# Performance work log

Hardware: AMD Instinct MI355X
Metric: run time of the kernel (lower is better)

## Reference

```python
import jax, jax.numpy as jnp
import numpy as np

DIM = 1024
NUM_EXPERTS = 8
HIDDEN = 4096
CAP_FACTOR = 2.0
B, S = 4, 2048


def setup_inputs() -> dict:
    key = jax.random.key(0)
    ks = jax.random.split(key, 6)
    scale_r = 1.0 / np.sqrt(DIM)
    scale_1 = 1.0 / np.sqrt(DIM)
    scale_2 = 1.0 / np.sqrt(HIDDEN)
    return {
        "x": jax.random.normal(ks[0], (B, S, DIM), dtype=jnp.float32),
        # router: nn.Linear(dim, num_experts, bias=False) -> weight [E, D]
        "router_w": jax.random.uniform(ks[1], (NUM_EXPERTS, DIM), jnp.float32, -scale_r, scale_r),
        # stacked expert MLP params
        "w1": jax.random.uniform(ks[2], (NUM_EXPERTS, DIM, HIDDEN), jnp.float32, -scale_1, scale_1),
        "b1": jax.random.uniform(ks[3], (NUM_EXPERTS, HIDDEN), jnp.float32, -scale_1, scale_1),
        "w2": jax.random.uniform(ks[4], (NUM_EXPERTS, HIDDEN, DIM), jnp.float32, -scale_2, scale_2),
        "b2": jax.random.uniform(ks[5], (NUM_EXPERTS, DIM), jnp.float32, -scale_2, scale_2),
    }


def reference(x, router_w, w1, b1, w2, b2):
    # x: [B, S, D]
    Bz, Sz, Dz = x.shape
    E = router_w.shape[0]
    capacity = max(1, int(Sz * CAP_FACTOR / E) + 1)

    # router softmax over experts: [B, S, E]
    scores = jax.nn.softmax(jnp.einsum("bsd,ed->bse", x, router_w), axis=-1)

    # expert-choice: each expert picks top-C tokens. [B, E, S] -> [B, E, C]
    scores_t = jnp.swapaxes(scores, 1, 2)
    gate_vals, sel_idx = jax.lax.top_k(scores_t, capacity)

    # gather selected tokens: [B, E, C, D]
    b_idx = jnp.arange(Bz)[:, None, None]
    tokens = x[b_idx, sel_idx]

    # batched expert MLP (GELU exact, matching nn.GELU default)
    h = jnp.einsum("becd,edh->bech", tokens, w1) + b1[None, :, None, :]
    h = jax.nn.gelu(h, approximate=False)
    y = jnp.einsum("bech,ehd->becd", h, w2) + b2[None, :, None, :]

    # gate and scatter-add combine back to [B, S, D]
    gated = y * gate_vals[..., None]
    out = jnp.zeros_like(x).at[b_idx, sel_idx].add(gated)
    return out
```

## Files before the change

kernel.cpp:

```cpp
#include <hip/hip_runtime.h>
#include <cstdint>

#define DIMD  1024
#define NEXP  8
#define HIDN  4096
#define BATCH 4
#define SEQ   2048
#define CAPC  513
#define RPEX  2176
#define TPEX  17
#define MTOT  (NEXP * RPEX)
#define MTILES (MTOT / 128)

typedef __bf16 bf16x8 __attribute__((ext_vector_type(8)));
typedef float  f32x4  __attribute__((ext_vector_type(4)));

__device__ __forceinline__ unsigned short f2bf(float f) {
    unsigned u = __float_as_uint(f);
    unsigned r = (u + 0x7FFFu + ((u >> 16) & 1u)) >> 16;
    return (unsigned short)r;
}

__device__ __forceinline__ void swz_grp(int GY, int& bx, int& by) {
    int xcd = blockIdx.x & 7, pos = blockIdx.x >> 3;
    int tps = TPEX * GY;
    int sc = pos / tps, rem = pos - sc * tps;
    int bxl = rem / GY, byIn = rem - bxl * GY;
    bx = xcd * TPEX + bxl;
    by = sc * GY + byIn;
}

__global__ __launch_bounds__(64)
void router_kernel(const float* __restrict__ x, const float* __restrict__ rw,
                   float* __restrict__ scores) {
    int token = blockIdx.x;
    int lane  = threadIdx.x;
    const float4* xr = reinterpret_cast<const float4*>(x + (size_t)token * DIMD);
    float4 xv[4];
#pragma unroll
    for (int j = 0; j < 4; ++j) xv[j] = xr[lane * 4 + j];
    float acc[NEXP];
#pragma unroll
    for (int e = 0; e < NEXP; ++e) {
        const float4* wr = reinterpret_cast<const float4*>(rw + (size_t)e * DIMD);
        float a = 0.f;
#pragma unroll
        for (int j = 0; j < 4; ++j) {
            float4 wv = wr[lane * 4 + j];
            a += xv[j].x * wv.x; a += xv[j].y * wv.y;
            a += xv[j].z * wv.z; a += xv[j].w * wv.w;
        }
#pragma unroll
        for (int off = 32; off > 0; off >>= 1) a += __shfl_xor(a, off);
        acc[e] = a;
    }
    float m = acc[0];
#pragma unroll
    for (int e = 1; e < NEXP; ++e) m = fmaxf(m, acc[e]);
    float s = 0.f;
#pragma unroll
    for (int e = 0; e < NEXP; ++e) { acc[e] = expf(acc[e] - m); s += acc[e]; }
    float inv = 1.f / s;
    if (lane == 0) {
        int b = token >> 11;
        int t = token & (SEQ - 1);
#pragma unroll
        for (int e = 0; e < NEXP; ++e)
            scores[((size_t)(b * NEXP + e)) * SEQ + t] = acc[e] * inv;
    }
}

__global__ __launch_bounds__(256)
void topk_kernel(const float* __restrict__ scores, int* __restrict__ sel,
                 float* __restrict__ gate, int* __restrict__ cnt,
                 int* __restrict__ invmap) {
    int be    = blockIdx.x >> 3;
    int chunk = blockIdx.x & 7;
    const float* sc = scores + (size_t)be * SEQ;
    __shared__ float s_sc[SEQ];
    int t = threadIdx.x;
#pragma unroll
    for (int q = 0; q < 8; ++q) s_sc[t + q * 256] = sc[t + q * 256];
    __syncthreads();
    int i = chunk * 256 + t;
    float v = s_sc[i];
    int r = 0;
#pragma unroll 8
    for (int j = 0; j < SEQ; ++j) {
        float u = s_sc[j];
        r += (u > v) || (u == v && j < i);
    }
    if (r < CAPC) {
        sel [(size_t)be * CAPC + r] = i;
        gate[(size_t)be * CAPC + r] = v;
        int b = be >> 3, e = be & 7;
        int tok = b * SEQ + i;
        int p = atomicAdd(cnt + tok, 1);
        invmap[(size_t)tok * 8 + p] = e * RPEX + b * CAPC + r;
    }
}

__global__ __launch_bounds__(256)
void gather_kernel(const float* __restrict__ x, const int* __restrict__ sel,
                   unsigned short* __restrict__ dhi) {
    int gr = blockIdx.x;
    int e  = gr / RPEX;
    int rl = gr - e * RPEX;
    int t  = threadIdx.x;
    size_t dbase = (size_t)gr * DIMD + t * 4;
    if (rl < BATCH * CAPC) {
        int b = rl / CAPC, c = rl - b * CAPC;
        int tok = sel[(size_t)(b * NEXP + e) * CAPC + c];
        float4 v = *reinterpret_cast<const float4*>(x + ((size_t)(b * SEQ + tok)) * DIMD + t * 4);
        ushort4 h;
        h.x = f2bf(v.x); h.y = f2bf(v.y); h.z = f2bf(v.z); h.w = f2bf(v.w);
        *reinterpret_cast<ushort4*>(dhi + dbase) = h;
    } else {
        ushort4 z = {0, 0, 0, 0};
        *reinterpret_cast<ushort4*>(dhi + dbase) = z;
    }
}

__global__ __launch_bounds__(256)
void convT_kernel(const float* __restrict__ src, unsigned short* __restrict__ dhi,
                  int Nsrc, size_t srcEStride, int k0, int n0, int kLen, int nLen) {
    int e = blockIdx.z;
    src += (size_t)e * srcEStride;
    dhi += (size_t)e * kLen * nLen;
    int kb = blockIdx.x * 64, nb = blockIdx.y * 64;
    __shared__ float T[64][65];
    int t = threadIdx.x;
    for (int i = t; i < 1024; i += 256) {
        int r = i >> 4, c4 = (i & 15) * 4;
        float4 v = *reinterpret_cast<const float4*>(
            src + (size_t)(k0 + kb + r) * Nsrc + n0 + nb + c4);
        T[r][c4 + 0] = v.x; T[r][c4 + 1] = v.y; T[r][c4 + 2] = v.z; T[r][c4 + 3] = v.w;
    }
    __syncthreads();
    for (int i = t; i < 1024; i += 256) {
        int n = i >> 4, kc = (i & 15) * 4;
        ushort4 h;
        h.x = f2bf(T[kc + 0][n]); h.y = f2bf(T[kc + 1][n]);
        h.z = f2bf(T[kc + 2][n]); h.w = f2bf(T[kc + 3][n]);
        *reinterpret_cast<ushort4*>(dhi + (size_t)(nb + n) * kLen + kb + kc) = h;
    }
}

#define GEMM_STAGE_DECLS \
    __shared__ __align__(16) unsigned short As_h[128][40]; \
    __shared__ __align__(16) unsigned short Bs_h[128][40];

__device__ __forceinline__ void mfma_single(f32x4 acc[4][4], const bf16x8 ah[4],
                                            const bf16x8 bh[4]) {
#pragma unroll
    for (int m = 0; m < 4; ++m)
#pragma unroll
        for (int n = 0; n < 4; ++n)
            acc[m][n] = __builtin_amdgcn_mfma_f32_16x16x32_bf16(ah[m], bh[n], acc[m][n], 0, 0, 0);
}

#define LOADK1(k0c) do { \
    rAh0 = *(const uint4*)(Ahi + a0 + (k0c) + kc0); rAh1 = *(const uint4*)(Ahi + a1 + (k0c) + kc0); \
    rBh0 = *(const uint4*)(Bh  + b0 + (k0c) + kc0); rBh1 = *(const uint4*)(Bh  + b1o + (k0c) + kc0); } while (0)

#define STAGEK1() do { \
    *(uint4*)&As_h[srow][kc0] = rAh0; *(uint4*)&As_h[srow + 64][kc0] = rAh1; \
    *(uint4*)&Bs_h[srow][kc0] = rBh0; *(uint4*)&Bs_h[srow + 64][kc0] = rBh1; } while (0)

#define FRAG_READS() \
    bf16x8 ah[4], bh[4]; \
    _Pragma("unroll") \
    for (int m = 0; m < 4; ++m) \
        ah[m] = *(const bf16x8*)&As_h[wr * 64 + m * 16 + li][grp * 8]; \
    _Pragma("unroll") \
    for (int n = 0; n < 4; ++n) \
        bh[n] = *(const bf16x8*)&Bs_h[wc * 64 + n * 16 + li][grp * 8];

__global__ __launch_bounds__(256)
void gemm1_mfma(const unsigned short* __restrict__ Ahi,
                const unsigned short* __restrict__ Whi,
                const float* __restrict__ bias, unsigned short* __restrict__ Hhi,
                size_t wstride, int nbias0, int ldh, int GY) {
    const int K = DIMD;
    int bx, by; swz_grp(GY, bx, by);
    int bn = by * 128;
    int e = bx / TPEX;
    const unsigned short* Bh = Whi + (size_t)e * wstride;
    int t = threadIdx.x;
    int l = t & 63, wid = t >> 6;
    int wr = wid >> 1, wc = wid & 1;
    int grp = l >> 4, li = l & 15;

    GEMM_STAGE_DECLS

    int srow = t >> 2, scg = t & 3, kc0 = scg * 8;
    size_t a0 = (size_t)(bx * 128 + srow) * K;
    size_t a1 = (size_t)(bx * 128 + srow + 64) * K;
    size_t b0 = (size_t)(bn + srow) * K;
    size_t b1o = (size_t)(bn + srow + 64) * K;

    f32x4 acc[4][4];
#pragma unroll
    for (int m = 0; m < 4; ++m)
#pragma unroll
        for (int n = 0; n < 4; ++n) { f32x4 z = {0.f, 0.f, 0.f, 0.f}; acc[m][n] = z; }

    uint4 rAh0, rAh1, rBh0, rBh1;
    LOADK1(0);
    for (int kt = 0; kt < K; kt += 32) {
        __syncthreads();
        STAGEK1();
        __syncthreads();
        if (kt + 32 < K) LOADK1(kt + 32);
        FRAG_READS();
        mfma_single(acc, ah, bh);
    }

    int hr0 = bx * 128 + wr * 64;
    int cb = bn + wc * 64;
#pragma unroll
    for (int m = 0; m < 4; ++m)
#pragma unroll
        for (int q = 0; q < 4; ++q) {
            int row = hr0 + m * 16 + grp * 4 + q;
#pragma unroll
            for (int n = 0; n < 4; ++n) {
                int col = cb + n * 16 + li;
                float v = acc[m][n][q] + bias[(size_t)e * HIDN + nbias0 + col];
                float g = 0.5f * v * (1.0f + erff(v * 0.70710678118654752f));
                Hhi[(size_t)row * ldh + col] = f2bf(g);
            }
        }
}

__global__ __launch_bounds__(256)
void gemm2_mfma(const unsigned short* __restrict__ Ahi,
                const unsigned short* __restrict__ Whi,
                const float* __restrict__ bias, const float* __restrict__ gate,
                float* __restrict__ Y, size_t wstride, int K, int GY) {
    int bx, by; swz_grp(GY, bx, by);
    int bn = by * 128;
    int e = bx / TPEX;
    int rbase_e = (bx - e * TPEX) * 128;
    const unsigned short* Bh = Whi + (size_t)e * wstride;
    int t = threadIdx.x;
    int l = t & 63, wid = t >> 6;
    int wr = wid >> 1, wc = wid & 1;
    int grp = l >> 4, li = l & 15;

    GEMM_STAGE_DECLS

    int srow = t >> 2, scg = t & 3, kc0 = scg * 8;
    size_t a0 = (size_t)(bx * 128 + srow) * K;
    size_t a1 = (size_t)(bx * 128 + srow + 64) * K;
    size_t b0 = (size_t)(bn + srow) * K;
    size_t b1o = (size_t)(bn + srow + 64) * K;

    f32x4 acc[4][4];
#pragma unroll
    for (int m = 0; m < 4; ++m)
#pragma unroll
        for (int n = 0; n < 4; ++n) { f32x4 z = {0.f, 0.f, 0.f, 0.f}; acc[m][n] = z; }

    uint4 rAh0, rAh1, rBh0, rBh1;
    LOADK1(0);
    for (int kt = 0; kt < K; kt += 32) {
        __syncthreads();
        STAGEK1();
        __syncthreads();
        if (kt + 32 < K) LOADK1(kt + 32);
        FRAG_READS();
        mfma_single(acc, ah, bh);
    }

    int cb = bn + wc * 64;
#pragma unroll
    for (int m = 0; m < 4; ++m)
#pragma unroll
        for (int q = 0; q < 4; ++q) {
            int off = wr * 64 + m * 16 + grp * 4 + q;
            int rloc = rbase_e + off;
            if (rloc < BATCH * CAPC) {
                int b = rloc / CAPC, c = rloc - b * CAPC;
                float g = gate[(size_t)(b * NEXP + e) * CAPC + c];
                size_t grow = (size_t)bx * 128 + off;
#pragma unroll
                for (int n = 0; n < 4; ++n) {
                    int col = cb + n * 16 + li;
                    float v = acc[m][n][q];
                    size_t yo = grow * DIMD + col;
                    if (bias) Y[yo] = g * (v + bias[(size_t)e * DIMD + col]);
                    else      Y[yo] = Y[yo] + g * v;
                }
            }
        }
}

__global__ __launch_bounds__(64)
void combine_kernel(const float* __restrict__ Y, const int* __restrict__ cnt,
                    const int* __restrict__ invmap, float* __restrict__ out) {
    int tok = blockIdx.x;
    int lane = threadIdx.x;
    int n = cnt[tok];
    f32x4 acc[4];
#pragma unroll
    for (int q = 0; q < 4; ++q) { f32x4 z = {0.f, 0.f, 0.f, 0.f}; acc[q] = z; }
#pragma unroll
    for (int j = 0; j < 8; ++j) {
        if (j < n) {
            int row = invmap[(size_t)tok * 8 + j];
            const f32x4* yr = reinterpret_cast<const f32x4*>(Y + (size_t)row * DIMD);
#pragma unroll
            for (int q = 0; q < 4; ++q) acc[q] += yr[q * 64 + lane];
        }
    }
    f32x4* op = reinterpret_cast<f32x4*>(out + (size_t)tok * DIMD);
#pragma unroll
    for (int q = 0; q < 4; ++q) op[q * 64 + lane] = acc[q];
}

extern "C" void kernel_launch(void* const* d_in, const int* in_sizes, int n_in,
                              void* d_out, int out_size, void* d_ws, size_t ws_size,
                              hipStream_t stream) {
    (void)in_sizes; (void)n_in; (void)out_size;
    const float* x  = (const float*)d_in[0];
    const float* rw = (const float*)d_in[1];
    const float* w1 = (const float*)d_in[2];
    const float* b1 = (const float*)d_in[3];
    const float* w2 = (const float*)d_in[4];
    const float* b2 = (const float*)d_in[5];
    float* out = (float*)d_out;

    char* ws = (char*)d_ws;
    size_t off = 0;
    auto alloc = [&](size_t bytes) -> char* {
        char* p = ws + off;
        off = (off + bytes + 255) & ~(size_t)255;
        return p;
    };

    float* scores = (float*)alloc((size_t)BATCH * NEXP * SEQ * 4);
    int*   sel    = (int*)  alloc((size_t)BATCH * NEXP * CAPC * 4);
    float* gate   = (float*)alloc((size_t)BATCH * NEXP * CAPC * 4);
    int*   cnt    = (int*)  alloc((size_t)BATCH * SEQ * 4);
    int*   invmap = (int*)  alloc((size_t)BATCH * SEQ * 8 * 4);
    float* Y      = (float*)alloc((size_t)MTOT * DIMD * 4);
    size_t common = off;

    const size_t A1B = (size_t)MTOT * DIMD * 2;
    int C = 8;
    for (int c = 1; c <= 8; c <<= 1) {
        size_t wc = (size_t)NEXP * (HIDN / c) * DIMD * 2;
        size_t hc = (size_t)MTOT * (HIDN / c) * 2;
        size_t need = common + A1B + 2 * wc + hc + (8u << 20);
        if (need <= ws_size) { C = c; break; }
    }
    const int HN = HIDN / C;
    const int nY1 = HN / 128;
    const int GY1 = (nY1 < 8) ? nY1 : 8;

    unsigned short* A1h = (unsigned short*)alloc(A1B);
    size_t WCB = (size_t)NEXP * HN * DIMD * 2;
    size_t HCB = (size_t)MTOT * HN * 2;
    unsigned short* W1h = (unsigned short*)alloc(WCB);
    unsigned short* W2h = (unsigned short*)alloc(WCB);
    unsigned short* Hh  = (unsigned short*)alloc(HCB);

    hipMemsetAsync(cnt, 0, (size_t)BATCH * SEQ * 4, stream);
    router_kernel<<<BATCH * SEQ, 64, 0, stream>>>(x, rw, scores);
    topk_kernel<<<BATCH * NEXP * 8, 256, 0, stream>>>(scores, sel, gate, cnt, invmap);
    gather_kernel<<<MTOT, 256, 0, stream>>>(x, sel, A1h);

    for (int c = 0; c < C; ++c) {
        convT_kernel<<<dim3(DIMD / 64, HN / 64, NEXP), 256, 0, stream>>>(
            w1, W1h, HIDN, (size_t)DIMD * HIDN, 0, c * HN, DIMD, HN);
        gemm1_mfma<<<MTILES * nY1, 256, 0, stream>>>(
            A1h, W1h, b1, Hh, (size_t)HN * DIMD, c * HN, HN, GY1);
        convT_kernel<<<dim3(HN / 64, DIMD / 64, NEXP), 256, 0, stream>>>(
            w2, W2h, DIMD, (size_t)HIDN * DIMD, c * HN, 0, HN, DIMD);
        gemm2_mfma<<<MTILES * (DIMD / 128), 256, 0, stream>>>(
            Hh, W2h, (c == 0) ? b2 : nullptr, gate, Y,
            (size_t)DIMD * HN, HN, 4);
    }
    combine_kernel<<<BATCH * SEQ, 64, 0, stream>>>(Y, cnt, invmap, out);
}
```

Measured before the change: 687.0 us.

## Use direct global-to-LDS loads with double-buffered, XOR-swizzled GEMM tiles

Replaces the register-staged shared-memory fill in both expert GEMMs with global_load_lds direct-to-LDS transfers into two ping-pong buffers. Fragment reads use an XOR swizzle instead of padded rows to avoid bank conflicts. This removes one barrier per K step and the register round trip, so the next tile's load overlaps the current MFMA work. It relies on the async-load intrinsic's lane-to-address mapping matching the swizzled layout, and on the single barrier after the MFMAs being sufficient to order the async LDS writes.

```diff
diff --git a/kernel.cpp b/kernel.cpp
--- a/kernel.cpp
+++ b/kernel.cpp
@@ -19,6 +19,12 @@
     unsigned u = __float_as_uint(f);
     unsigned r = (u + 0x7FFFu + ((u >> 16) & 1u)) >> 16;
     return (unsigned short)r;
+}
+
+__device__ __forceinline__ void gl16(const unsigned short* g, unsigned short* l) {
+    __builtin_amdgcn_global_load_lds(
+        (const __attribute__((address_space(1))) void*)g,
+        (__attribute__((address_space(3))) void*)l, 16, 0, 0);
 }
 
 __device__ __forceinline__ void swz_grp(int GY, int& bx, int& by) {
@@ -146,35 +152,57 @@
     }
 }
 
-#define GEMM_STAGE_DECLS \
-    __shared__ __align__(16) unsigned short As_h[128][40]; \
-    __shared__ __align__(16) unsigned short Bs_h[128][40];
-
-__device__ __forceinline__ void mfma_single(f32x4 acc[4][4], const bf16x8 ah[4],
-                                            const bf16x8 bh[4]) {
-#pragma unroll
-    for (int m = 0; m < 4; ++m)
-#pragma unroll
-        for (int n = 0; n < 4; ++n)
-            acc[m][n] = __builtin_amdgcn_mfma_f32_16x16x32_bf16(ah[m], bh[n], acc[m][n], 0, 0, 0);
-}
-
-#define LOADK1(k0c) do { \
-    rAh0 = *(const uint4*)(Ahi + a0 + (k0c) + kc0); rAh1 = *(const uint4*)(Ahi + a1 + (k0c) + kc0); \
-    rBh0 = *(const uint4*)(Bh  + b0 + (k0c) + kc0); rBh1 = *(const uint4*)(Bh  + b1o + (k0c) + kc0); } while (0)
-
-#define STAGEK1() do { \
-    *(uint4*)&As_h[srow][kc0] = rAh0; *(uint4*)&As_h[srow + 64][kc0] = rAh1; \
-    *(uint4*)&Bs_h[srow][kc0] = rBh0; *(uint4*)&Bs_h[srow + 64][kc0] = rBh1; } while (0)
-
-#define FRAG_READS() \
-    bf16x8 ah[4], bh[4]; \
-    _Pragma("unroll") \
-    for (int m = 0; m < 4; ++m) \
-        ah[m] = *(const bf16x8*)&As_h[wr * 64 + m * 16 + li][grp * 8]; \
-    _Pragma("unroll") \
-    for (int n = 0; n < 4; ++n) \
-        bh[n] = *(const bf16x8*)&Bs_h[wc * 64 + n * 16 + li][grp * 8];
+
+#define GEMM_PRE(Abase, Bbase, Kc)                                              \
+    int t = threadIdx.x;                                                        \
+    int l = t & 63, wid = t >> 6;                                               \
+    int wr = wid >> 1, wc = wid & 1;                                            \
+    int grp = l >> 4, li = l & 15;                                              \
+    int fsw  = (grp ^ ((li >> 1) & 3)) * 8;         \
+    int gsrc = ((l & 3) ^ ((l >> 3) & 3)) * 8;      \
+    int ra0 = (wid * 2) * 16 + (l >> 2);          \
+    int ra1 = ra0 + 16;                                                         \
+    __shared__ __align__(16) unsigned short As[2][4096];                        \
+    __shared__ __align__(16) unsigned short Bs[2][4096];                        \
+    int regA = wid * 1024;                            \
+    const unsigned short* gA0 = (Abase) + (size_t)(bx * 128 + ra0) * (Kc) + gsrc; \
+    const unsigned short* gA1 = (Abase) + (size_t)(bx * 128 + ra1) * (Kc) + gsrc; \
+    const unsigned short* gB0 = (Bbase) + (size_t)(bn + ra0) * (Kc) + gsrc;     \
+    const unsigned short* gB1 = (Bbase) + (size_t)(bn + ra1) * (Kc) + gsrc;     \
+    f32x4 acc[4][4];                                                            \
+    _Pragma("unroll")                                                           \
+    for (int m = 0; m < 4; ++m)                                                 \
+        _Pragma("unroll")                                                       \
+        for (int n = 0; n < 4; ++n) { f32x4 z = {0.f,0.f,0.f,0.f}; acc[m][n] = z; }
+
+#define STAGE(buf, kt) do {                                                     \
+    gl16(gA0 + (kt), &As[buf][regA]);                                           \
+    gl16(gA1 + (kt), &As[buf][regA + 512]);                                     \
+    gl16(gB0 + (kt), &Bs[buf][regA]);                                           \
+    gl16(gB1 + (kt), &Bs[buf][regA + 512]); } while (0)
+
+#define GEMM_LOOP(Kc) do {                                                      \
+    STAGE(0, 0);                                                                \
+    __syncthreads();                                                            \
+    int cur = 0;                                                                \
+    for (int kt = 0; kt < (Kc); kt += 32) {                                     \
+        if (kt + 32 < (Kc)) STAGE(cur ^ 1, kt + 32);                            \
+        bf16x8 ah[4], bh[4];                                                    \
+        const unsigned short* aB = &As[cur][wr * 2048 + li * 32 + fsw];         \
+        const unsigned short* bB = &Bs[cur][wc * 2048 + li * 32 + fsw];         \
+        ah[0] = *(const bf16x8*)(aB);        ah[1] = *(const bf16x8*)(aB + 512); \
+        ah[2] = *(const bf16x8*)(aB + 1024); ah[3] = *(const bf16x8*)(aB + 1536); \
+        bh[0] = *(const bf16x8*)(bB);        bh[1] = *(const bf16x8*)(bB + 512); \
+        bh[2] = *(const bf16x8*)(bB + 1024); bh[3] = *(const bf16x8*)(bB + 1536); \
+        _Pragma("unroll")                                                       \
+        for (int m = 0; m < 4; ++m)                                             \
+            _Pragma("unroll")                                                   \
+            for (int n = 0; n < 4; ++n)                                         \
+                acc[m][n] = __builtin_amdgcn_mfma_f32_16x16x32_bf16(            \
+                    ah[m], bh[n], acc[m][n], 0, 0, 0);                          \
+        __syncthreads();                                                        \
+        cur ^= 1;                                                               \
+    } } while (0)
 
 __global__ __launch_bounds__(256)
 void gemm1_mfma(const unsigned short* __restrict__ Ahi,
@@ -186,35 +214,9 @@
     int bn = by * 128;
     int e = bx / TPEX;
     const unsigned short* Bh = Whi + (size_t)e * wstride;
-    int t = threadIdx.x;
-    int l = t & 63, wid = t >> 6;
-    int wr = wid >> 1, wc = wid & 1;
-    int grp = l >> 4, li = l & 15;
-
-    GEMM_STAGE_DECLS
-
-    int srow = t >> 2, scg = t & 3, kc0 = scg * 8;
-    size_t a0 = (size_t)(bx * 128 + srow) * K;
-    size_t a1 = (size_t)(bx * 128 + srow + 64) * K;
-    size_t b0 = (size_t)(bn + srow) * K;
-    size_t b1o = (size_t)(bn + srow + 64) * K;
-
-    f32x4 acc[4][4];
-#pragma unroll
-    for (int m = 0; m < 4; ++m)
-#pragma unroll
-        for (int n = 0; n < 4; ++n) { f32x4 z = {0.f, 0.f, 0.f, 0.f}; acc[m][n] = z; }
-
-    uint4 rAh0, rAh1, rBh0, rBh1;
-    LOADK1(0);
-    for (int kt = 0; kt < K; kt += 32) {
-        __syncthreads();
-        STAGEK1();
-        __syncthreads();
-        if (kt + 32 < K) LOADK1(kt + 32);
-        FRAG_READS();
-        mfma_single(acc, ah, bh);
-    }
+
+    GEMM_PRE(Ahi, Bh, K)
+    GEMM_LOOP(K);
 
     int hr0 = bx * 128 + wr * 64;
     int cb = bn + wc * 64;
@@ -243,35 +245,9 @@
     int e = bx / TPEX;
     int rbase_e = (bx - e * TPEX) * 128;
     const unsigned short* Bh = Whi + (size_t)e * wstride;
-    int t = threadIdx.x;
-    int l = t & 63, wid = t >> 6;
-    int wr = wid >> 1, wc = wid & 1;
-    int grp = l >> 4, li = l & 15;
-
-    GEMM_STAGE_DECLS
-
-    int srow = t >> 2, scg = t & 3, kc0 = scg * 8;
-    size_t a0 = (size_t)(bx * 128 + srow) * K;
-    size_t a1 = (size_t)(bx * 128 + srow + 64) * K;
-    size_t b0 = (size_t)(bn + srow) * K;
-    size_t b1o = (size_t)(bn + srow + 64) * K;
-
-    f32x4 acc[4][4];
-#pragma unroll
-    for (int m = 0; m < 4; ++m)
-#pragma unroll
-        for (int n = 0; n < 4; ++n) { f32x4 z = {0.f, 0.f, 0.f, 0.f}; acc[m][n] = z; }
-
-    uint4 rAh0, rAh1, rBh0, rBh1;
-    LOADK1(0);
-    for (int kt = 0; kt < K; kt += 32) {
-        __syncthreads();
-        STAGEK1();
-        __syncthreads();
-        if (kt + 32 < K) LOADK1(kt + 32);
-        FRAG_READS();
-        mfma_single(acc, ah, bh);
-    }
+
+    GEMM_PRE(Ahi, Bh, K)
+    GEMM_LOOP(K);
 
     int cb = bn + wc * 64;
 #pragma unroll
```

Measured after the change: 650.9 us. 1.06x faster.
